# Performance work log

Hardware: AMD Instinct MI355X
Metric: run time of the kernel (lower is better)

Reference implementation:

```python
import jax, jax.numpy as jnp
import numpy as np

NUM_LEVELS = 16
FEATS_PER_LEVEL = 2
LOG2_HASHMAP = 19
TABLE_SIZE = 1 << LOG2_HASHMAP
BASE_RES = 16
DESIRED_RES = 4096
PER_LEVEL_SCALE = float(np.exp(np.log(DESIRED_RES / BASE_RES) / (NUM_LEVELS - 1)))
PRIMES = (np.uint32(1), np.uint32(2654435761), np.uint32(805459861))
N_POINTS = 2_000_000


def _level_features(x, table, level):
    # x: [N,3] in [0,1]; table: [TABLE_SIZE, F]
    scale = BASE_RES * (PER_LEVEL_SCALE ** level) - 1.0
    res = int(np.ceil(scale)) + 1
    dense = (res ** 3) <= TABLE_SIZE  # tcnn uses dense indexing when grid fits
    pos = x * scale + 0.5
    pos0 = jnp.floor(pos)
    w = pos - pos0                     # trilinear weights, [N,3]
    base = pos0.astype(jnp.uint32)
    out = jnp.zeros((x.shape[0], table.shape[1]), dtype=table.dtype)
    for c in range(8):                 # 8 corners of the voxel
        offs = [(c >> d) & 1 for d in range(3)]
        pc = [jnp.minimum(base[:, d] + np.uint32(offs[d]), np.uint32(res - 1)) for d in range(3)]
        if dense:
            idx = pc[0] + pc[1] * np.uint32(res) + pc[2] * np.uint32(res * res)
        else:
            idx = (pc[0] * PRIMES[0]) ^ (pc[1] * PRIMES[1]) ^ (pc[2] * PRIMES[2])
            idx = idx & np.uint32(TABLE_SIZE - 1)
        wt = jnp.ones(x.shape[0], dtype=x.dtype)
        for d in range(3):
            wt = wt * (w[:, d] if offs[d] else (1.0 - w[:, d]))
        out = out + wt[:, None] * table[idx.astype(jnp.int32)]
    return out


def hashgrid_encode(x, tables):
    # x: [N,3] in [0,1]; tables: [L, TABLE_SIZE, F] -> [N, L*F]
    return jnp.concatenate(
        [_level_features(x, tables[l], l) for l in range(NUM_LEVELS)], axis=-1)


def setup_inputs() -> dict:
    key = jax.random.key(0)
    k1, k2, k3, k4, k5 = jax.random.split(key, 5)
    points = jax.random.uniform(k1, (N_POINTS, 3), dtype=jnp.float32)
    # tcnn hashgrid init: uniform(-1e-4, 1e-4)
    tables = jax.random.uniform(k2, (NUM_LEVELS, TABLE_SIZE, FEATS_PER_LEVEL),
                                minval=-1e-4, maxval=1e-4, dtype=jnp.float32)
    def kaiming(k, fan_out, fan_in):
        bound = np.sqrt(2.0) * np.sqrt(3.0 / fan_in)
        return jax.random.uniform(k, (fan_out, fan_in), minval=-bound, maxval=bound,
                                  dtype=jnp.float32)
    W1 = kaiming(k3, 32, 32)
    W2 = kaiming(k4, 32, 32)
    W3 = kaiming(k5, 4, 32)
    aabb = jnp.stack([jnp.zeros(3, jnp.float32), jnp.ones(3, jnp.float32)])
    return {"points": points, "tables": tables, "W1": W1, "W2": W2, "W3": W3,
            "aabb": aabb}


def reference(points, tables, W1, W2, W3, aabb):
    texc = jnp.clip((points - aabb[0][None, :]) / (aabb[1] - aabb[0])[None, :], 0.0, 1.0)
    enc = hashgrid_encode(texc, tables)            # [N, 32]
    h = jax.nn.relu(enc @ W1.T)
    h = jax.nn.relu(h @ W2.T)
    out = h @ W3.T                                 # [N, 4]
    mn = jnp.array([0.0, 0.0, 0.0, 0.01], dtype=out.dtype)
    mx = jnp.array([1.0, 1.0, 1.0, 1.0], dtype=out.dtype)
    return jax.nn.sigmoid(out) * (mx - mn) + mn
```

## Files before the change

kernel.cpp:

```cpp
#include <hip/hip_runtime.h>
#include <cmath>


namespace {
constexpr int kLevels = 16;
constexpr unsigned kTableSize = 1u << 19;
constexpr unsigned kMask = kTableSize - 1u;

typedef _Float16 half2_t __attribute__((ext_vector_type(2)));
typedef unsigned int u32;

struct LevelParams {
  float scale[kLevels];
  unsigned res[kLevels];
  int dense[kLevels];
};
}

__global__ __launch_bounds__(256)
void conv_tables_kernel(const float2* __restrict__ src, half2_t* __restrict__ dst,
                        int n_entries,
                        const float* __restrict__ W1, const float* __restrict__ W2,
                        const float* __restrict__ W3, half2_t* __restrict__ Wh)
{
  int i = blockIdx.x * blockDim.x + threadIdx.x;
  if (i < 512) {
    Wh[i] = half2_t{(_Float16)W1[2 * i], (_Float16)W1[2 * i + 1]};
  } else if (i < 1024) {
    int t = i - 512;
    Wh[512 + t] = half2_t{(_Float16)W2[2 * t], (_Float16)W2[2 * t + 1]};
  } else if (i < 1088) {
    int t = i - 1024;
    Wh[1024 + t] = half2_t{(_Float16)W3[2 * t], (_Float16)W3[2 * t + 1]};
  }
  int stride = gridDim.x * blockDim.x;
  for (; i < n_entries; i += stride) {
    float2 v = src[i];
    dst[i] = half2_t{(_Float16)v.x, (_Float16)v.y};
  }
}

__device__ __forceinline__ u32 sel4(uint4 v, u32 j) {
  u32 lo = (j & 1u) ? v.y : v.x;
  u32 hi = (j & 1u) ? v.w : v.z;
  return (j & 2u) ? hi : lo;
}

__global__ __launch_bounds__(256)
void encode_kernel(const float* __restrict__ points,
                   const u32* __restrict__ tables,
                   const float* __restrict__ aabb,
                   half2_t* __restrict__ enc,
                   LevelParams lp, int n, int bpl)
{
  int l = blockIdx.x / bpl;
  int i = (blockIdx.x - l * bpl) * blockDim.x + threadIdx.x;
  if (i >= n) return;

  float a0x = aabb[0], a0y = aabb[1], a0z = aabb[2];
  float a1x = aabb[3], a1y = aabb[4], a1z = aabb[5];
  float x = fminf(fmaxf((points[3 * i + 0] - a0x) / (a1x - a0x), 0.f), 1.f);
  float y = fminf(fmaxf((points[3 * i + 1] - a0y) / (a1y - a0y), 0.f), 1.f);
  float z = fminf(fmaxf((points[3 * i + 2] - a0z) / (a1z - a0z), 0.f), 1.f);

  float s = lp.scale[l];
  unsigned res = lp.res[l];
  bool dense = (lp.dense[l] != 0);
  unsigned rm1 = res - 1u;
  unsigned res2 = res * res;
  const u32* tab = tables + (size_t)l * kTableSize;

  float fx = x * s + 0.5f, fy = y * s + 0.5f, fz = z * s + 0.5f;
  float fx0 = floorf(fx), fy0 = floorf(fy), fz0 = floorf(fz);
  float wx = fx - fx0, wy = fy - fy0, wz = fz - fz0;
  unsigned bx = (unsigned)fx0, by = (unsigned)fy0, bz = (unsigned)fz0;

  unsigned pcx0 = min(bx, rm1), pcx1 = min(bx + 1u, rm1);

  u32 idx0[4], idx1[4];
  #pragma unroll
  for (int p = 0; p < 4; ++p) {
    unsigned oy = (unsigned)(p & 1);
    unsigned oz = (unsigned)(p >> 1);
    unsigned pcy = min(by + oy, rm1);
    unsigned pcz = min(bz + oz, rm1);
    if (dense) {
      u32 b = pcy * res + pcz * res2;
      idx0[p] = pcx0 + b;
      idx1[p] = pcx1 + b;
    } else {
      u32 h = (pcy * 2654435761u) ^ (pcz * 805459861u);
      idx0[p] = (pcx0 ^ h) & kMask;
      idx1[p] = (pcx1 ^ h) & kMask;
    }
  }

  uint4 v[4];
  #pragma unroll
  for (int p = 0; p < 4; ++p)
    v[p] = *reinterpret_cast<const uint4*>(tab + (idx0[p] & ~3u));

  u32 e1x[4] = {0u, 0u, 0u, 0u};
  #pragma unroll
  for (int p = 0; p < 4; ++p) {
    if ((idx0[p] ^ idx1[p]) >= 4u) e1x[p] = tab[idx1[p]];
  }

  float wx1 = wx, wx0 = 1.f - wx;
  float acc0 = 0.f, acc1 = 0.f;
  #pragma unroll
  for (int p = 0; p < 4; ++p) {
    unsigned oy = (unsigned)(p & 1);
    unsigned oz = (unsigned)(p >> 1);
    float wyz = (oy ? wy : 1.f - wy) * (oz ? wz : 1.f - wz);
    u32 e0 = sel4(v[p], idx0[p] & 3u);
    u32 e1g = sel4(v[p], idx1[p] & 3u);
    u32 e1 = ((idx0[p] ^ idx1[p]) < 4u) ? e1g : e1x[p];
    half2_t f0 = __builtin_bit_cast(half2_t, e0);
    half2_t f1 = __builtin_bit_cast(half2_t, e1);
    float w0 = wyz * wx0, w1 = wyz * wx1;
    acc0 += w0 * (float)f0.x + w1 * (float)f1.x;
    acc1 += w0 * (float)f0.y + w1 * (float)f1.y;
  }
  enc[(size_t)l * n + i] = half2_t{(_Float16)acc0, (_Float16)acc1};
}

__device__ __forceinline__ float dot2_acc(half2_t a, half2_t b, float c) {
#if __has_builtin(__builtin_amdgcn_fdot2)
  return __builtin_amdgcn_fdot2(a, b, c, false);
#else
  return c + (float)a.x * (float)b.x + (float)a.y * (float)b.y;
#endif
}

__global__ __launch_bounds__(256)
void mlp_kernel(const half2_t* __restrict__ enc,
                const half2_t* __restrict__ Wh,
                float* __restrict__ out, int n)
{
  int i = blockIdx.x * blockDim.x + threadIdx.x;
  if (i >= n) return;

  half2_t e[16];
  #pragma unroll
  for (int l = 0; l < kLevels; ++l) e[l] = enc[(size_t)l * n + i];

  const half2_t* W1h = Wh;
  const half2_t* W2h = Wh + 512;
  const half2_t* W3h = Wh + 1024;

  float h1f[32];
  #pragma unroll
  for (int j = 0; j < 32; ++j) {
    float acc = 0.f;
    #pragma unroll
    for (int k = 0; k < 16; ++k) acc = dot2_acc(e[k], W1h[16 * j + k], acc);
    h1f[j] = fmaxf(acc, 0.f);
  }
  half2_t h1[16];
  #pragma unroll
  for (int k = 0; k < 16; ++k)
    h1[k] = half2_t{(_Float16)h1f[2 * k], (_Float16)h1f[2 * k + 1]};

  float h2f[32];
  #pragma unroll
  for (int j = 0; j < 32; ++j) {
    float acc = 0.f;
    #pragma unroll
    for (int k = 0; k < 16; ++k) acc = dot2_acc(h1[k], W2h[16 * j + k], acc);
    h2f[j] = fmaxf(acc, 0.f);
  }
  half2_t h2[16];
  #pragma unroll
  for (int k = 0; k < 16; ++k)
    h2[k] = half2_t{(_Float16)h2f[2 * k], (_Float16)h2f[2 * k + 1]};

  float o[4];
  #pragma unroll
  for (int j = 0; j < 4; ++j) {
    float acc = 0.f;
    #pragma unroll
    for (int k = 0; k < 16; ++k) acc = dot2_acc(h2[k], W3h[16 * j + k], acc);
    o[j] = acc;
  }

  float4 r;
  r.x = 1.f / (1.f + __expf(-o[0]));
  r.y = 1.f / (1.f + __expf(-o[1]));
  r.z = 1.f / (1.f + __expf(-o[2]));
  r.w = 0.99f / (1.f + __expf(-o[3])) + 0.01f;
  reinterpret_cast<float4*>(out)[i] = r;
}

__global__ __launch_bounds__(256)
void hashgrid_mlp_kernel(const float* __restrict__ points,
                         const float* __restrict__ tables,
                         const float* __restrict__ W1,
                         const float* __restrict__ W2,
                         const float* __restrict__ W3,
                         const float* __restrict__ aabb,
                         float* __restrict__ out,
                         LevelParams lp, int n)
{
  int i = blockIdx.x * blockDim.x + threadIdx.x;
  if (i >= n) return;
  float a0x = aabb[0], a0y = aabb[1], a0z = aabb[2];
  float a1x = aabb[3], a1y = aabb[4], a1z = aabb[5];
  float x = fminf(fmaxf((points[3 * i + 0] - a0x) / (a1x - a0x), 0.f), 1.f);
  float y = fminf(fmaxf((points[3 * i + 1] - a0y) / (a1y - a0y), 0.f), 1.f);
  float z = fminf(fmaxf((points[3 * i + 2] - a0z) / (a1z - a0z), 0.f), 1.f);
  float enc[2 * kLevels];
  #pragma unroll
  for (int l = 0; l < kLevels; ++l) {
    float s = lp.scale[l];
    unsigned res = lp.res[l];
    bool dense = (lp.dense[l] != 0);
    unsigned rm1 = res - 1u;
    unsigned res2 = res * res;
    float fx = x * s + 0.5f, fy = y * s + 0.5f, fz = z * s + 0.5f;
    float fx0 = floorf(fx), fy0 = floorf(fy), fz0 = floorf(fz);
    float wx = fx - fx0, wy = fy - fy0, wz = fz - fz0;
    unsigned bx = (unsigned)fx0, by = (unsigned)fy0, bz = (unsigned)fz0;
    const float2* tab = reinterpret_cast<const float2*>(tables) + (size_t)l * kTableSize;
    float acc0 = 0.f, acc1 = 0.f;
    #pragma unroll
    for (int c = 0; c < 8; ++c) {
      unsigned ox = (unsigned)(c & 1);
      unsigned oy = (unsigned)((c >> 1) & 1);
      unsigned oz = (unsigned)((c >> 2) & 1);
      unsigned pcx = min(bx + ox, rm1);
      unsigned pcy = min(by + oy, rm1);
      unsigned pcz = min(bz + oz, rm1);
      unsigned idx;
      if (dense) idx = pcx + pcy * res + pcz * res2;
      else idx = (pcx ^ (pcy * 2654435761u) ^ (pcz * 805459861u)) & kMask;
      float wt = (ox ? wx : 1.f - wx) * (oy ? wy : 1.f - wy) * (oz ? wz : 1.f - wz);
      float2 f = tab[idx];
      acc0 += wt * f.x;
      acc1 += wt * f.y;
    }
    enc[2 * l + 0] = acc0;
    enc[2 * l + 1] = acc1;
  }
  float h1[32];
  #pragma unroll
  for (int j = 0; j < 32; ++j) {
    float acc = 0.f;
    #pragma unroll
    for (int k = 0; k < 32; ++k) acc += enc[k] * W1[32 * j + k];
    h1[j] = fmaxf(acc, 0.f);
  }
  float h2[32];
  #pragma unroll
  for (int j = 0; j < 32; ++j) {
    float acc = 0.f;
    #pragma unroll
    for (int k = 0; k < 32; ++k) acc += h1[k] * W2[32 * j + k];
    h2[j] = fmaxf(acc, 0.f);
  }
  float o[4];
  #pragma unroll
  for (int j = 0; j < 4; ++j) {
    float acc = 0.f;
    #pragma unroll
    for (int k = 0; k < 32; ++k) acc += h2[k] * W3[32 * j + k];
    o[j] = acc;
  }
  float4 r;
  r.x = 1.f / (1.f + __expf(-o[0]));
  r.y = 1.f / (1.f + __expf(-o[1]));
  r.z = 1.f / (1.f + __expf(-o[2]));
  r.w = 0.99f / (1.f + __expf(-o[3])) + 0.01f;
  reinterpret_cast<float4*>(out)[i] = r;
}

extern "C" void kernel_launch(void* const* d_in, const int* in_sizes, int n_in,
                              void* d_out, int out_size, void* d_ws, size_t ws_size,
                              hipStream_t stream) {
  const float* points = (const float*)d_in[0];
  const float* tables = (const float*)d_in[1];
  const float* W1     = (const float*)d_in[2];
  const float* W2     = (const float*)d_in[3];
  const float* W3     = (const float*)d_in[4];
  const float* aabb   = (const float*)d_in[5];
  float* out = (float*)d_out;
  int n = in_sizes[0] / 3;

  LevelParams lp;
  const double pls = std::exp(std::log(4096.0 / 16.0) / 15.0);
  for (int l = 0; l < kLevels; ++l) {
    double s = 16.0 * std::pow(pls, (double)l) - 1.0;
    lp.scale[l] = (float)s;
    long long res = (long long)std::ceil(s) + 1;
    lp.res[l] = (unsigned)res;
    lp.dense[l] = (res * res * res <= (long long)kTableSize) ? 1 : 0;
  }

  const int block = 256;
  const size_t tab_f16_bytes = (size_t)kLevels * kTableSize * sizeof(half2_t);
  const size_t enc_bytes     = (size_t)kLevels * (size_t)n * sizeof(half2_t);
  const size_t w_bytes       = 1088 * sizeof(half2_t);
  const size_t needed = tab_f16_bytes + enc_bytes + w_bytes;

  if (ws_size >= needed) {
    half2_t* tab_f16 = reinterpret_cast<half2_t*>(d_ws);
    half2_t* enc = reinterpret_cast<half2_t*>((char*)d_ws + tab_f16_bytes);
    half2_t* Wh  = reinterpret_cast<half2_t*>((char*)d_ws + tab_f16_bytes + enc_bytes);

    const int n_entries = kLevels * (int)kTableSize;
    conv_tables_kernel<<<2048, block, 0, stream>>>(
        reinterpret_cast<const float2*>(tables), tab_f16, n_entries, W1, W2, W3, Wh);

    const int bpl = (n + block - 1) / block;
    encode_kernel<<<bpl * kLevels, block, 0, stream>>>(
        points, reinterpret_cast<const u32*>(tab_f16), aabb, enc, lp, n, bpl);

    mlp_kernel<<<(n + block - 1) / block, block, 0, stream>>>(enc, Wh, out, n);
  } else {
    const int grid = (n + block - 1) / block;
    hashgrid_mlp_kernel<<<grid, block, 0, stream>>>(
        points, tables, W1, W2, W3, aabb, out, lp, n);
  }
}
```

Baseline: 770.3 us.

## Spatially sort points into 32^3 cells before hashgrid encoding

Adds a counting sort of points by coarse 32^3 voxel cell (histogram, scan, atomic scatter) so the encode kernel processes spatially coherent points and its table gathers hit cache better. The sorted points are staged in the output buffer, and the MLP writes results back through a permutation array. This adds several extra kernels, global atomics, a single-block scan and a scattered output write in exchange for better gather locality.

```diff
diff --git a/kernel.cpp b/kernel.cpp
--- a/kernel.cpp
+++ b/kernel.cpp
@@ -6,6 +6,7 @@
 constexpr int kLevels = 16;
 constexpr unsigned kTableSize = 1u << 19;
 constexpr unsigned kMask = kTableSize - 1u;
+constexpr int kCells = 32768;
 
 typedef _Float16 half2_t __attribute__((ext_vector_type(2)));
 typedef unsigned int u32;
@@ -40,6 +41,82 @@
   }
 }
 
+__device__ __forceinline__ void texc_of(const float* __restrict__ pts,
+                                        const float* __restrict__ aabb, int i,
+                                        float& x, float& y, float& z)
+{
+  float a0x = aabb[0], a0y = aabb[1], a0z = aabb[2];
+  float a1x = aabb[3], a1y = aabb[4], a1z = aabb[5];
+  x = fminf(fmaxf((pts[3 * i + 0] - a0x) / (a1x - a0x), 0.f), 1.f);
+  y = fminf(fmaxf((pts[3 * i + 1] - a0y) / (a1y - a0y), 0.f), 1.f);
+  z = fminf(fmaxf((pts[3 * i + 2] - a0z) / (a1z - a0z), 0.f), 1.f);
+}
+
+__device__ __forceinline__ int cell_of(float x, float y, float z)
+{
+  int cx = min((int)(x * 32.f), 31);
+  int cy = min((int)(y * 32.f), 31);
+  int cz = min((int)(z * 32.f), 31);
+  return cx + (cy << 5) + (cz << 10);
+}
+
+__global__ __launch_bounds__(256)
+void zero_hist_kernel(u32* __restrict__ hist)
+{
+  int i = blockIdx.x * blockDim.x + threadIdx.x;
+  if (i < kCells) hist[i] = 0u;
+}
+
+__global__ __launch_bounds__(256)
+void hist_kernel(const float* __restrict__ points, const float* __restrict__ aabb,
+                 u32* __restrict__ hist, int n)
+{
+  int i = blockIdx.x * blockDim.x + threadIdx.x;
+  if (i >= n) return;
+  float x, y, z;
+  texc_of(points, aabb, i, x, y, z);
+  atomicAdd(&hist[cell_of(x, y, z)], 1u);
+}
+
+__global__ __launch_bounds__(1024)
+void scan_kernel(const u32* __restrict__ hist, u32* __restrict__ cstart)
+{
+  __shared__ u32 sm[1024];
+  int t = threadIdx.x;
+  u32 loc[32];
+  u32 s = 0;
+  #pragma unroll
+  for (int k = 0; k < 32; ++k) { loc[k] = hist[t * 32 + k]; s += loc[k]; }
+  sm[t] = s;
+  __syncthreads();
+  u32 v = s;
+  for (int off = 1; off < 1024; off <<= 1) {
+    u32 a = (t >= off) ? sm[t - off] : 0u;
+    __syncthreads();
+    v += a;
+    sm[t] = v;
+    __syncthreads();
+  }
+  u32 run = v - s;
+  #pragma unroll
+  for (int k = 0; k < 32; ++k) { cstart[t * 32 + k] = run; run += loc[k]; }
+}
+
+__global__ __launch_bounds__(256)
+void scatter_kernel(const float* __restrict__ points, const float* __restrict__ aabb,
+                    u32* __restrict__ cstart, float4* __restrict__ sorted,
+                    u32* __restrict__ perm, int n)
+{
+  int i = blockIdx.x * blockDim.x + threadIdx.x;
+  if (i >= n) return;
+  float x, y, z;
+  texc_of(points, aabb, i, x, y, z);
+  int c = cell_of(x, y, z);
+  u32 slot = atomicAdd(&cstart[c], 1u);
+  sorted[slot] = float4{x, y, z, 0.f};
+  perm[slot] = (u32)i;
+}
+
 __device__ __forceinline__ u32 sel4(uint4 v, u32 j) {
   u32 lo = (j & 1u) ? v.y : v.x;
   u32 hi = (j & 1u) ? v.w : v.z;
@@ -47,9 +124,8 @@
 }
 
 __global__ __launch_bounds__(256)
-void encode_kernel(const float* __restrict__ points,
+void encode_kernel(const float4* __restrict__ pts,
                    const u32* __restrict__ tables,
-                   const float* __restrict__ aabb,
                    half2_t* __restrict__ enc,
                    LevelParams lp, int n, int bpl)
 {
@@ -57,11 +133,8 @@
   int i = (blockIdx.x - l * bpl) * blockDim.x + threadIdx.x;
   if (i >= n) return;
 
-  float a0x = aabb[0], a0y = aabb[1], a0z = aabb[2];
-  float a1x = aabb[3], a1y = aabb[4], a1z = aabb[5];
-  float x = fminf(fmaxf((points[3 * i + 0] - a0x) / (a1x - a0x), 0.f), 1.f);
-  float y = fminf(fmaxf((points[3 * i + 1] - a0y) / (a1y - a0y), 0.f), 1.f);
-  float z = fminf(fmaxf((points[3 * i + 2] - a0z) / (a1z - a0z), 0.f), 1.f);
+  float4 p = pts[i];
+  float x = p.x, y = p.y, z = p.z;
 
   float s = lp.scale[l];
   unsigned res = lp.res[l];
@@ -79,43 +152,114 @@
 
   u32 idx0[4], idx1[4];
   #pragma unroll
-  for (int p = 0; p < 4; ++p) {
-    unsigned oy = (unsigned)(p & 1);
-    unsigned oz = (unsigned)(p >> 1);
+  for (int q = 0; q < 4; ++q) {
+    unsigned oy = (unsigned)(q & 1);
+    unsigned oz = (unsigned)(q >> 1);
     unsigned pcy = min(by + oy, rm1);
     unsigned pcz = min(bz + oz, rm1);
     if (dense) {
       u32 b = pcy * res + pcz * res2;
-      idx0[p] = pcx0 + b;
-      idx1[p] = pcx1 + b;
+      idx0[q] = pcx0 + b;
+      idx1[q] = pcx1 + b;
     } else {
       u32 h = (pcy * 2654435761u) ^ (pcz * 805459861u);
-      idx0[p] = (pcx0 ^ h) & kMask;
-      idx1[p] = (pcx1 ^ h) & kMask;
+      idx0[q] = (pcx0 ^ h) & kMask;
+      idx1[q] = (pcx1 ^ h) & kMask;
     }
   }
 
   uint4 v[4];
   #pragma unroll
-  for (int p = 0; p < 4; ++p)
-    v[p] = *reinterpret_cast<const uint4*>(tab + (idx0[p] & ~3u));
+  for (int q = 0; q < 4; ++q)
+    v[q] = *reinterpret_cast<const uint4*>(tab + (idx0[q] & ~3u));
 
   u32 e1x[4] = {0u, 0u, 0u, 0u};
   #pragma unroll
-  for (int p = 0; p < 4; ++p) {
-    if ((idx0[p] ^ idx1[p]) >= 4u) e1x[p] = tab[idx1[p]];
+  for (int q = 0; q < 4; ++q) {
+    if ((idx0[q] ^ idx1[q]) >= 4u) e1x[q] = tab[idx1[q]];
   }
 
   float wx1 = wx, wx0 = 1.f - wx;
   float acc0 = 0.f, acc1 = 0.f;
   #pragma unroll
-  for (int p = 0; p < 4; ++p) {
-    unsigned oy = (unsigned)(p & 1);
-    unsigned oz = (unsigned)(p >> 1);
+  for (int q = 0; q < 4; ++q) {
+    unsigned oy = (unsigned)(q & 1);
+    unsigned oz = (unsigned)(q >> 1);
     float wyz = (oy ? wy : 1.f - wy) * (oz ? wz : 1.f - wz);
-    u32 e0 = sel4(v[p], idx0[p] & 3u);
-    u32 e1g = sel4(v[p], idx1[p] & 3u);
-    u32 e1 = ((idx0[p] ^ idx1[p]) < 4u) ? e1g : e1x[p];
+    u32 e0 = sel4(v[q], idx0[q] & 3u);
+    u32 e1g = sel4(v[q], idx1[q] & 3u);
+    u32 e1 = ((idx0[q] ^ idx1[q]) < 4u) ? e1g : e1x[q];
+    half2_t f0 = __builtin_bit_cast(half2_t, e0);
+    half2_t f1 = __builtin_bit_cast(half2_t, e1);
+    float w0 = wyz * wx0, w1 = wyz * wx1;
+    acc0 += w0 * (float)f0.x + w1 * (float)f1.x;
+    acc1 += w0 * (float)f0.y + w1 * (float)f1.y;
+  }
+  enc[(size_t)l * n + i] = half2_t{(_Float16)acc0, (_Float16)acc1};
+}
+
+__global__ __launch_bounds__(256)
+void encode_raw_kernel(const float* __restrict__ points,
+                       const u32* __restrict__ tables,
+                       const float* __restrict__ aabb,
+                       half2_t* __restrict__ enc,
+                       LevelParams lp, int n, int bpl)
+{
+  int l = blockIdx.x / bpl;
+  int i = (blockIdx.x - l * bpl) * blockDim.x + threadIdx.x;
+  if (i >= n) return;
+  float x, y, z;
+  texc_of(points, aabb, i, x, y, z);
+
+  float s = lp.scale[l];
+  unsigned res = lp.res[l];
+  bool dense = (lp.dense[l] != 0);
+  unsigned rm1 = res - 1u;
+  unsigned res2 = res * res;
+  const u32* tab = tables + (size_t)l * kTableSize;
+
+  float fx = x * s + 0.5f, fy = y * s + 0.5f, fz = z * s + 0.5f;
+  float fx0 = floorf(fx), fy0 = floorf(fy), fz0 = floorf(fz);
+  float wx = fx - fx0, wy = fy - fy0, wz = fz - fz0;
+  unsigned bx = (unsigned)fx0, by = (unsigned)fy0, bz = (unsigned)fz0;
+  unsigned pcx0 = min(bx, rm1), pcx1 = min(bx + 1u, rm1);
+
+  u32 idx0[4], idx1[4];
+  #pragma unroll
+  for (int q = 0; q < 4; ++q) {
+    unsigned oy = (unsigned)(q & 1);
+    unsigned oz = (unsigned)(q >> 1);
+    unsigned pcy = min(by + oy, rm1);
+    unsigned pcz = min(bz + oz, rm1);
+    if (dense) {
+      u32 b = pcy * res + pcz * res2;
+      idx0[q] = pcx0 + b;
+      idx1[q] = pcx1 + b;
+    } else {
+      u32 h = (pcy * 2654435761u) ^ (pcz * 805459861u);
+      idx0[q] = (pcx0 ^ h) & kMask;
+      idx1[q] = (pcx1 ^ h) & kMask;
+    }
+  }
+  uint4 v[4];
+  #pragma unroll
+  for (int q = 0; q < 4; ++q)
+    v[q] = *reinterpret_cast<const uint4*>(tab + (idx0[q] & ~3u));
+  u32 e1x[4] = {0u, 0u, 0u, 0u};
+  #pragma unroll
+  for (int q = 0; q < 4; ++q) {
+    if ((idx0[q] ^ idx1[q]) >= 4u) e1x[q] = tab[idx1[q]];
+  }
+  float wx1 = wx, wx0 = 1.f - wx;
+  float acc0 = 0.f, acc1 = 0.f;
+  #pragma unroll
+  for (int q = 0; q < 4; ++q) {
+    unsigned oy = (unsigned)(q & 1);
+    unsigned oz = (unsigned)(q >> 1);
+    float wyz = (oy ? wy : 1.f - wy) * (oz ? wz : 1.f - wz);
+    u32 e0 = sel4(v[q], idx0[q] & 3u);
+    u32 e1g = sel4(v[q], idx1[q] & 3u);
+    u32 e1 = ((idx0[q] ^ idx1[q]) < 4u) ? e1g : e1x[q];
     half2_t f0 = __builtin_bit_cast(half2_t, e0);
     half2_t f1 = __builtin_bit_cast(half2_t, e1);
     float w0 = wyz * wx0, w1 = wyz * wx1;
@@ -136,10 +280,13 @@
 __global__ __launch_bounds__(256)
 void mlp_kernel(const half2_t* __restrict__ enc,
                 const half2_t* __restrict__ Wh,
+                const u32* __restrict__ perm,
                 float* __restrict__ out, int n)
 {
   int i = blockIdx.x * blockDim.x + threadIdx.x;
   if (i >= n) return;
+
+  u32 orig = perm ? perm[i] : (u32)i;
 
   half2_t e[16];
   #pragma unroll
@@ -189,7 +336,7 @@
   r.y = 1.f / (1.f + __expf(-o[1]));
   r.z = 1.f / (1.f + __expf(-o[2]));
   r.w = 0.99f / (1.f + __expf(-o[3])) + 0.01f;
-  reinterpret_cast<float4*>(out)[i] = r;
+  reinterpret_cast<float4*>(out)[orig] = r;
 }
 
 __global__ __launch_bounds__(256)
@@ -204,11 +351,8 @@
 {
   int i = blockIdx.x * blockDim.x + threadIdx.x;
   if (i >= n) return;
-  float a0x = aabb[0], a0y = aabb[1], a0z = aabb[2];
-  float a1x = aabb[3], a1y = aabb[4], a1z = aabb[5];
-  float x = fminf(fmaxf((points[3 * i + 0] - a0x) / (a1x - a0x), 0.f), 1.f);
-  float y = fminf(fmaxf((points[3 * i + 1] - a0y) / (a1y - a0y), 0.f), 1.f);
-  float z = fminf(fmaxf((points[3 * i + 2] - a0z) / (a1z - a0z), 0.f), 1.f);
+  float x, y, z;
+  texc_of(points, aabb, i, x, y, z);
   float enc[2 * kLevels];
   #pragma unroll
   for (int l = 0; l < kLevels; ++l) {
@@ -297,28 +441,51 @@
   }
 
   const int block = 256;
+  const int n_entries = kLevels * (int)kTableSize;
   const size_t tab_f16_bytes = (size_t)kLevels * kTableSize * sizeof(half2_t);
   const size_t enc_bytes     = (size_t)kLevels * (size_t)n * sizeof(half2_t);
   const size_t w_bytes       = 1088 * sizeof(half2_t);
-  const size_t needed = tab_f16_bytes + enc_bytes + w_bytes;
-
-  if (ws_size >= needed) {
+  const size_t perm_bytes    = (size_t)n * sizeof(u32);
+  const size_t hist_bytes    = (size_t)kCells * sizeof(u32);
+
+  const size_t need_old    = tab_f16_bytes + enc_bytes + w_bytes;
+  const size_t need_sorted = need_old + perm_bytes + 2 * hist_bytes;
+  const bool out_fits_sorted = (size_t)out_size >= (size_t)n * sizeof(float4);
+
+  const int grid_n = (n + block - 1) / block;
+  const int bpl = grid_n;
+
+  if (ws_size >= need_sorted && out_fits_sorted) {
+    char* p = (char*)d_ws;
+    half2_t* tab_f16 = (half2_t*)p;               p += tab_f16_bytes;
+    half2_t* enc     = (half2_t*)p;               p += enc_bytes;
+    u32*     perm    = (u32*)p;                   p += perm_bytes;
+    u32*     hist    = (u32*)p;                   p += hist_bytes;
+    u32*     cstart  = (u32*)p;                   p += hist_bytes;
+    half2_t* Wh      = (half2_t*)p;
+    float4*  sorted  = (float4*)d_out;
+
+    conv_tables_kernel<<<2048, block, 0, stream>>>(
+        reinterpret_cast<const float2*>(tables), tab_f16, n_entries, W1, W2, W3, Wh);
+    zero_hist_kernel<<<(kCells + block - 1) / block, block, 0, stream>>>(hist);
+    hist_kernel<<<grid_n, block, 0, stream>>>(points, aabb, hist, n);
+    scan_kernel<<<1, 1024, 0, stream>>>(hist, cstart);
+    scatter_kernel<<<grid_n, block, 0, stream>>>(points, aabb, cstart, sorted, perm, n);
+    encode_kernel<<<bpl * kLevels, block, 0, stream>>>(
+        sorted, reinterpret_cast<const u32*>(tab_f16), enc, lp, n, bpl);
+    mlp_kernel<<<grid_n, block, 0, stream>>>(enc, Wh, perm, out, n);
+  } else if (ws_size >= need_old) {
     half2_t* tab_f16 = reinterpret_cast<half2_t*>(d_ws);
     half2_t* enc = reinterpret_cast<half2_t*>((char*)d_ws + tab_f16_bytes);
     half2_t* Wh  = reinterpret_cast<half2_t*>((char*)d_ws + tab_f16_bytes + enc_bytes);
 
-    const int n_entries = kLevels * (int)kTableSize;
     conv_tables_kernel<<<2048, block, 0, stream>>>(
         reinterpret_cast<const float2*>(tables), tab_f16, n_entries, W1, W2, W3, Wh);
-
-    const int bpl = (n + block - 1) / block;
-    encode_kernel<<<bpl * kLevels, block, 0, stream>>>(
+    encode_raw_kernel<<<bpl * kLevels, block, 0, stream>>>(
         points, reinterpret_cast<const u32*>(tab_f16), aabb, enc, lp, n, bpl);
-
-    mlp_kernel<<<(n + block - 1) / block, block, 0, stream>>>(enc, Wh, out, n);
+    mlp_kernel<<<grid_n, block, 0, stream>>>(enc, Wh, nullptr, out, n);
   } else {
-    const int grid = (n + block - 1) / block;
-    hashgrid_mlp_kernel<<<grid, block, 0, stream>>>(
+    hashgrid_mlp_kernel<<<grid_n, block, 0, stream>>>(
         points, tables, W1, W2, W3, aabb, out, lp, n);
   }
 }
```

After: 770.1 us. No clear change (-0.0%).
